# Performance work log

Measured on AMD Instinct MI355X. Metric: run time of the kernel, lower is better.

The kernel has to match this reference:

```python
import jax, jax.numpy as jnp
import numpy as np

# Fixed hyperparameters matching init_kwargs
DIL_START = 2
DIL_END = 1024   # n_dilations = 1022
N_BULGE = 2
BATCH, L, C = 8, 2048, 4


def _variant_tables():
    """Static (forward_shift, backward_shift, has_GU) table, one row per output feature.
    Order per distance s: [main AU_CG+GU, left bulge d=1..n, right bulge d=1..n]."""
    f, b, g = [], [], []
    for s in range(DIL_START, DIL_END):
        f.append(s + 1); b.append(s + 1); g.append(1.0)            # dilate
        for d in range(1, N_BULGE + 1):                            # left bulge
            f.append(s + 1); b.append(s + 1 + d); g.append(0.0)
        for d in range(1, N_BULGE + 1):                            # right bulge
            f.append(s + 1 + d); b.append(s + 1); g.append(0.0)
    return np.array(f), np.array(b), np.array(g, dtype=np.float32)


def setup_inputs() -> dict:
    key = jax.random.key(0)
    x = jax.random.uniform(key, (BATCH, L, C), dtype=jnp.float32)
    return {"x": x}


def reference(x) -> jnp.ndarray:
    n, L_, _ = x.shape
    f_np, b_np, g_np = _variant_tables()
    f_arr = jnp.asarray(f_np)
    b_arr = jnp.asarray(b_np)
    gu_arr = jnp.asarray(g_np).astype(x.dtype)
    max_f = int(f_np.max())
    max_b = int(b_np.max())

    # y[i] = x[i+f] (zeros past the end);  z[i] = x[i-b] (zeros before start)
    xp_r = jnp.pad(x, ((0, 0), (0, max_f), (0, 0)))
    xp_l = jnp.pad(x, ((0, 0), (max_b, 0), (0, 0)))
    w4 = jnp.array([2.0, 3.0, 3.0, 2.0], dtype=x.dtype)  # AU/CG pairing weights

    def variant(f, b, g):
        y = jax.lax.dynamic_slice_in_dim(xp_r, f, L_, axis=1)          # (n, L, 4)
        z = jax.lax.dynamic_slice_in_dim(xp_l, max_b - b, L_, axis=1)  # (n, L, 4)
        # base: sum_c w[c] * x[i+f, c] * x[i-b, 3-c]  (reverse-complement correlation)
        base = jnp.einsum('nlc,nlc->nl', y * w4, z[..., ::-1])
        # GU wobble pairs (channels 2,3), weight 2, only for the non-bulge variant
        gu = 2.0 * (y[..., 2] * z[..., 3] + y[..., 3] * z[..., 2])
        return base + g * gu

    out = jax.vmap(variant)(f_arr, b_arr, gu_arr)  # (F, n, L)
    return jnp.transpose(out, (1, 2, 0))           # (n, L, F)
```

## Files before the change

### kernel.cpp

```cpp
#include <hip/hip_runtime.h>

#define LSEQ 2048
#define NS   1022
#define NF   5110
#define NB   8
#define IT   128
#define TPB  256

__device__ __forceinline__ float4 zero4() { return make_float4(0.f, 0.f, 0.f, 0.f); }

__device__ __forceinline__ float basescore(const float4 y, const float4 z) {
    return 2.f * y.x * z.w + 3.f * y.y * z.z + 3.f * y.z * z.y + 2.f * y.w * z.x;
}

__global__ __launch_bounds__(TPB) void fdcnn_kernel(const float4* __restrict__ x,
                                                    float* __restrict__ out) {
    __shared__ float4 xs[LSEQ];
    const int n = blockIdx.z;
    const float4* xg = x + (size_t)n * LSEQ;
    #pragma unroll
    for (int k = 0; k < LSEQ / TPB; ++k)
        xs[threadIdx.x + k * TPB] = xg[threadIdx.x + k * TPB];
    __syncthreads();

    const int sidx = blockIdx.x * TPB + threadIdx.x;
    if (sidx >= NS) return;
    const int s = sidx + 2;
    const int i0 = blockIdx.y * IT;

    float* op = out + ((size_t)n * LSEQ + i0) * (size_t)NF + (size_t)sidx * 5;

    float4 yA, yB, zA, zB;
    {
        int p = i0 + s + 1;
        yA = xs[p & (LSEQ - 1)]; if (p >= LSEQ) yA = zero4();
        p = i0 + s + 2;
        yB = xs[p & (LSEQ - 1)]; if (p >= LSEQ) yB = zero4();
        int q = i0 - s - 3;
        zA = xs[q & (LSEQ - 1)]; if (q < 0) zA = zero4();
        q = i0 - s - 2;
        zB = xs[q & (LSEQ - 1)]; if (q < 0) zB = zero4();
    }

    #pragma unroll 8
    for (int ii = 0; ii < IT; ++ii) {
        const int i = i0 + ii;

        int p = i + s + 3;
        float4 yC = xs[p & (LSEQ - 1)]; if (p >= LSEQ) yC = zero4();
        int q = i - s - 1;
        float4 zC = xs[q & (LSEQ - 1)]; if (q < 0) zC = zero4();

        const float4 y1 = yA, y2 = yB, y3 = yC;
        const float4 z3 = zA, z2 = zB, z1 = zC;

        float o0 = basescore(y1, z1) + 2.f * (y1.z * z1.w + y1.w * z1.z);
        float o1 = basescore(y1, z2);
        float o2 = basescore(y1, z3);
        float o3 = basescore(y2, z1);
        float o4 = basescore(y3, z1);

        op[0] = o0; op[1] = o1; op[2] = o2; op[3] = o3; op[4] = o4;
        op += NF;

        yA = yB; yB = yC;
        zA = zB; zB = zC;
    }
}

extern "C" void kernel_launch(void* const* d_in, const int* in_sizes, int n_in,
                              void* d_out, int out_size, void* d_ws, size_t ws_size,
                              hipStream_t stream) {
    const float4* x = (const float4*)d_in[0];
    float* out = (float*)d_out;
    dim3 grid((NS + TPB - 1) / TPB, LSEQ / IT, NB);
    dim3 block(TPB);
    fdcnn_kernel<<<grid, block, 0, stream>>>(x, out);
}
```

Before: 75.60 us.

## Stage outputs in shared memory and write coalesced float4 rows

Each thread now writes its five feature values for four consecutive positions into a shared-memory tile instead of storing them straight to global memory, where neighbouring threads were five floats apart. After a barrier, the block writes the tile out as contiguous float4 stores, with a tail path for the partial last feature block. This targets poor store coalescing on a large, write-bound output. The cost is extra LDS traffic, two block barriers per four rows, and float4 stores that are only 8-byte aligned on odd rows because the row length is 5110.

Result: faster. 72.81 us (-3.7%).

```diff
diff --git a/kernel.cpp b/kernel.cpp
--- a/kernel.cpp
+++ b/kernel.cpp
@@ -5,7 +5,9 @@
 #define NF   5110
 #define NB   8
 #define IT   128
+#define GI   4
 #define TPB  256
+#define FPB  (TPB * 5)
 
 __device__ __forceinline__ float4 zero4() { return make_float4(0.f, 0.f, 0.f, 0.f); }
 
@@ -16,19 +18,20 @@
 __global__ __launch_bounds__(TPB) void fdcnn_kernel(const float4* __restrict__ x,
                                                     float* __restrict__ out) {
     __shared__ float4 xs[LSEQ];
+    __shared__ float st[GI][FPB];
+
+    const int t = threadIdx.x;
     const int n = blockIdx.z;
     const float4* xg = x + (size_t)n * LSEQ;
     #pragma unroll
     for (int k = 0; k < LSEQ / TPB; ++k)
-        xs[threadIdx.x + k * TPB] = xg[threadIdx.x + k * TPB];
+        xs[t + k * TPB] = xg[t + k * TPB];
     __syncthreads();
 
-    const int sidx = blockIdx.x * TPB + threadIdx.x;
-    if (sidx >= NS) return;
+    const int sidx = blockIdx.x * TPB + t;
     const int s = sidx + 2;
     const int i0 = blockIdx.y * IT;
-
-    float* op = out + ((size_t)n * LSEQ + i0) * (size_t)NF + (size_t)sidx * 5;
+    const int fbase = blockIdx.x * FPB;
 
     float4 yA, yB, zA, zB;
     {
@@ -42,29 +45,48 @@
         zB = xs[q & (LSEQ - 1)]; if (q < 0) zB = zero4();
     }
 
-    #pragma unroll 8
-    for (int ii = 0; ii < IT; ++ii) {
-        const int i = i0 + ii;
+    for (int gb = 0; gb < IT / GI; ++gb) {
+        #pragma unroll
+        for (int ig = 0; ig < GI; ++ig) {
+            const int i = i0 + gb * GI + ig;
 
-        int p = i + s + 3;
-        float4 yC = xs[p & (LSEQ - 1)]; if (p >= LSEQ) yC = zero4();
-        int q = i - s - 1;
-        float4 zC = xs[q & (LSEQ - 1)]; if (q < 0) zC = zero4();
+            int p = i + s + 3;
+            float4 yC = xs[p & (LSEQ - 1)]; if (p >= LSEQ) yC = zero4();
+            int q = i - s - 1;
+            float4 zC = xs[q & (LSEQ - 1)]; if (q < 0) zC = zero4();
 
-        const float4 y1 = yA, y2 = yB, y3 = yC;
-        const float4 z3 = zA, z2 = zB, z1 = zC;
+            const float4 y1 = yA, y2 = yB, y3 = yC;
+            const float4 z3 = zA, z2 = zB, z1 = zC;
 
-        float o0 = basescore(y1, z1) + 2.f * (y1.z * z1.w + y1.w * z1.z);
-        float o1 = basescore(y1, z2);
-        float o2 = basescore(y1, z3);
-        float o3 = basescore(y2, z1);
-        float o4 = basescore(y3, z1);
+            float* sp = &st[ig][t * 5];
+            sp[0] = basescore(y1, z1) + 2.f * (y1.z * z1.w + y1.w * z1.z);
+            sp[1] = basescore(y1, z2);
+            sp[2] = basescore(y1, z3);
+            sp[3] = basescore(y2, z1);
+            sp[4] = basescore(y3, z1);
 
-        op[0] = o0; op[1] = o1; op[2] = o2; op[3] = o3; op[4] = o4;
-        op += NF;
+            yA = yB; yB = yC;
+            zA = zB; zB = zC;
+        }
+        __syncthreads();
 
-        yA = yB; yB = yC;
-        zA = zB; zB = zC;
+        const size_t obase = ((size_t)n * LSEQ + (i0 + gb * GI)) * (size_t)NF;
+        #pragma unroll
+        for (int k = 0; k < 5; ++k) {
+            const int v  = k * TPB + t;
+            const int ig = v / 320;
+            const int fo = (v - ig * 320) * 4;
+            const int rem = NF - (fbase + fo);
+            const float4 val = *(const float4*)&st[ig][fo];
+            float* dst = out + obase + (size_t)ig * NF + fbase + fo;
+            if (rem >= 4) {
+                *(float4*)dst = val;
+            } else if (rem > 0) {
+                dst[0] = val.x;
+                if (rem > 1) dst[1] = val.y;
+            }
+        }
+        __syncthreads();
     }
 }
 
```

## Assign four shifts per thread with vectorized float4 output stores

Applied to the files above, without the earlier changes.

Each thread now computes four consecutive shift distances (twenty contiguous features) per position and writes them with float4 stores instead of scalar stores. Shared-memory staging is removed and x is read directly from global memory through a register sliding window. The tile along the sequence shrinks and the grid is reorganized so one block covers all shifts. The float4 stores may be misaligned on rows where the row stride is not a multiple of four floats.

After: 172.5 us. 2.28x slower.

```diff
diff --git a/kernel.cpp b/kernel.cpp
--- a/kernel.cpp
+++ b/kernel.cpp
@@ -4,67 +4,75 @@
 #define NS   1022
 #define NF   5110
 #define NB   8
-#define IT   128
+#define IT   16
 #define TPB  256
 
-__device__ __forceinline__ float4 zero4() { return make_float4(0.f, 0.f, 0.f, 0.f); }
+__device__ __forceinline__ float cscore(const float4 y, const float4 z) {
+    return 2.f * y.x * z.w + 3.f * y.y * z.z + 3.f * y.z * z.y + 2.f * y.w * z.x;
+}
 
-__device__ __forceinline__ float basescore(const float4 y, const float4 z) {
-    return 2.f * y.x * z.w + 3.f * y.y * z.z + 3.f * y.z * z.y + 2.f * y.w * z.x;
+__device__ __forceinline__ float4 loadx(const float4* __restrict__ xg, int p) {
+    int pc = p < 0 ? 0 : (p > LSEQ - 1 ? LSEQ - 1 : p);
+    float4 v = xg[pc];
+    if ((unsigned)p >= (unsigned)LSEQ) v = make_float4(0.f, 0.f, 0.f, 0.f);
+    return v;
 }
 
 __global__ __launch_bounds__(TPB) void fdcnn_kernel(const float4* __restrict__ x,
                                                     float* __restrict__ out) {
-    __shared__ float4 xs[LSEQ];
-    const int n = blockIdx.z;
+    const int gl = threadIdx.x;
+    const int slane = 4 * gl + 2;
+    const int fbase = gl * 20;
+    const int i0 = blockIdx.x * IT;
+    const int n  = blockIdx.y;
     const float4* xg = x + (size_t)n * LSEQ;
+
+    float4 Y[6], Z[6];
     #pragma unroll
-    for (int k = 0; k < LSEQ / TPB; ++k)
-        xs[threadIdx.x + k * TPB] = xg[threadIdx.x + k * TPB];
-    __syncthreads();
-
-    const int sidx = blockIdx.x * TPB + threadIdx.x;
-    if (sidx >= NS) return;
-    const int s = sidx + 2;
-    const int i0 = blockIdx.y * IT;
-
-    float* op = out + ((size_t)n * LSEQ + i0) * (size_t)NF + (size_t)sidx * 5;
-
-    float4 yA, yB, zA, zB;
-    {
-        int p = i0 + s + 1;
-        yA = xs[p & (LSEQ - 1)]; if (p >= LSEQ) yA = zero4();
-        p = i0 + s + 2;
-        yB = xs[p & (LSEQ - 1)]; if (p >= LSEQ) yB = zero4();
-        int q = i0 - s - 3;
-        zA = xs[q & (LSEQ - 1)]; if (q < 0) zA = zero4();
-        q = i0 - s - 2;
-        zB = xs[q & (LSEQ - 1)]; if (q < 0) zB = zero4();
+    for (int d = 0; d < 6; ++d) {
+        Y[d] = loadx(xg, i0 + slane + 1 + d);
+        Z[d] = loadx(xg, i0 - slane - 1 - d);
     }
 
-    #pragma unroll 8
+    float* orow = out + ((size_t)n * LSEQ + i0) * (size_t)NF + fbase;
+    const bool full = (fbase + 20) <= NF;
+
+    #pragma unroll 4
     for (int ii = 0; ii < IT; ++ii) {
-        const int i = i0 + ii;
+        float o[4][5];
+        #pragma unroll
+        for (int k = 0; k < 4; ++k) {
+            o[k][0] = cscore(Y[k], Z[k]) + 2.f * (Y[k].z * Z[k].w + Y[k].w * Z[k].z);
+            o[k][1] = cscore(Y[k],     Z[k + 1]);
+            o[k][2] = cscore(Y[k],     Z[k + 2]);
+            o[k][3] = cscore(Y[k + 1], Z[k]);
+            o[k][4] = cscore(Y[k + 2], Z[k]);
+        }
 
-        int p = i + s + 3;
-        float4 yC = xs[p & (LSEQ - 1)]; if (p >= LSEQ) yC = zero4();
-        int q = i - s - 1;
-        float4 zC = xs[q & (LSEQ - 1)]; if (q < 0) zC = zero4();
+        if (full) {
+            #pragma unroll
+            for (int m = 0; m < 5; ++m) {
+                const float4 v = make_float4(o[(4*m+0)/5][(4*m+0)%5],
+                                             o[(4*m+1)/5][(4*m+1)%5],
+                                             o[(4*m+2)/5][(4*m+2)%5],
+                                             o[(4*m+3)/5][(4*m+3)%5]);
+                *(float4*)(orow + 4 * m) = v;
+            }
+        } else {
+            *(float4*)(orow + 0) = make_float4(o[0][0], o[0][1], o[0][2], o[0][3]);
+            *(float4*)(orow + 4) = make_float4(o[0][4], o[1][0], o[1][1], o[1][2]);
+            *(float2*)(orow + 8) = make_float2(o[1][3], o[1][4]);
+        }
 
-        const float4 y1 = yA, y2 = yB, y3 = yC;
-        const float4 z3 = zA, z2 = zB, z1 = zC;
+        const int inext = i0 + ii + 1;
+        #pragma unroll
+        for (int d = 0; d < 5; ++d) Y[d] = Y[d + 1];
+        Y[5] = loadx(xg, inext + slane + 6);
+        #pragma unroll
+        for (int d = 5; d > 0; --d) Z[d] = Z[d - 1];
+        Z[0] = loadx(xg, inext - slane - 1);
 
-        float o0 = basescore(y1, z1) + 2.f * (y1.z * z1.w + y1.w * z1.z);
-        float o1 = basescore(y1, z2);
-        float o2 = basescore(y1, z3);
-        float o3 = basescore(y2, z1);
-        float o4 = basescore(y3, z1);
-
-        op[0] = o0; op[1] = o1; op[2] = o2; op[3] = o3; op[4] = o4;
-        op += NF;
-
-        yA = yB; yB = yC;
-        zA = zB; zB = zC;
+        orow += NF;
     }
 }
 
@@ -73,7 +81,7 @@
                               hipStream_t stream) {
     const float4* x = (const float4*)d_in[0];
     float* out = (float*)d_out;
-    dim3 grid((NS + TPB - 1) / TPB, LSEQ / IT, NB);
+    dim3 grid(LSEQ / IT, NB);
     dim3 block(TPB);
     fdcnn_kernel<<<grid, block, 0, stream>>>(x, out);
 }
```
